# Kernel tuning notes

Hardware: AMD Instinct MI355X
Metric: run time of the kernel (lower is better)

Reference implementation:

```python
import jax, jax.numpy as jnp
from jax import lax
import numpy as np

ALPHA = 100.0  # NetVLAD beta

def _avg_pool2(x):
    # AvgPool2d(2, stride=2) on NCHW
    s = lax.reduce_window(x, 0.0, lax.add, (1, 1, 2, 2), (1, 1, 2, 2), 'VALID')
    return s * 0.25

def _conv3x3(x, w, b):
    y = lax.conv_general_dilated(x, w, (1, 1), 'SAME',
                                 dimension_numbers=('NCHW', 'OIHW', 'NCHW'))
    return y + b[None, :, None, None]

def _l2norm(v, axis):
    return v / jnp.maximum(jnp.linalg.norm(v, axis=axis, keepdims=True), 1e-12)


def setup_inputs() -> dict:
    key = jax.random.key(0)
    ks = jax.random.split(key, 10)
    N, H, W = 16, 512, 512
    K, D = 64, 16          # clusters, NetVLAD feature dim (conv2 out channels)
    T, E, Hd = 64, 300, 512  # caption len, emb dim (rnn_inp=rnn_out), rnn_hid
    img = jax.random.normal(ks[0], (N, 3, H, W), jnp.float32)
    cap = jax.random.normal(ks[1], (N, T, E), jnp.float32)
    conv1_w = jax.random.normal(ks[2], (4, 3, 3, 3), jnp.float32) * 0.1
    conv1_b = jnp.zeros((4,), jnp.float32)
    conv2_w = jax.random.normal(ks[3], (16, 4, 3, 3), jnp.float32) * 0.1
    conv2_b = jnp.zeros((16,), jnp.float32)
    centroids = jax.random.uniform(ks[4], (K, D), jnp.float32)  # torch.rand init
    nv_w = 2.0 * ALPHA * centroids                     # 1x1 conv weight, squeezed [K,D]
    nv_b = -ALPHA * jnp.linalg.norm(centroids, axis=1)  # [K]
    fc_w = jax.random.normal(ks[5], (Hd, K * D), jnp.float32) * 0.02
    fc_b = jnp.zeros((Hd,), jnp.float32)
    hid_w = jax.random.normal(ks[6], (Hd, E + Hd), jnp.float32) * 0.02
    hid_b = jnp.zeros((Hd,), jnp.float32)
    out_w = jax.random.normal(ks[7], (E, Hd), jnp.float32) * 0.02
    out_b = jnp.zeros((E,), jnp.float32)
    return dict(img=img, cap=cap, conv1_w=conv1_w, conv1_b=conv1_b,
                conv2_w=conv2_w, conv2_b=conv2_b, centroids=centroids,
                nv_w=nv_w, nv_b=nv_b, fc_w=fc_w, fc_b=fc_b,
                hid_w=hid_w, hid_b=hid_b, out_w=out_w, out_b=out_b)


def reference(img, cap, conv1_w, conv1_b, conv2_w, conv2_b, centroids,
              nv_w, nv_b, fc_w, fc_b, hid_w, hid_b, out_w, out_b):
    # CNN encoder
    x = jax.nn.relu(_conv3x3(img, conv1_w, conv1_b))
    x = _avg_pool2(x)
    x = jax.nn.relu(_conv3x3(x, conv2_w, conv2_b))
    x = _avg_pool2(x)                      # [N, 16, 128, 128]
    N, C = x.shape[0], x.shape[1]
    xf = x.reshape(N, C, -1)               # [N, C, HW]
    # NetVLAD: 1x1 conv -> softmax over clusters
    soft_assign = jnp.einsum('kc,nch->nkh', nv_w, xf) + nv_b[None, :, None]
    soft_assign = jax.nn.softmax(soft_assign, axis=1)  # [N, K, HW]
    # algebraic two-matmul form of sum_hw a[n,k,hw]*(x[n,c,hw]-centroids[k,c])
    a_sum = soft_assign.sum(axis=-1)                      # [N, K]
    vlad = jnp.einsum('nkh,nch->nkc', soft_assign, xf)    # [N, K, C]
    vlad = vlad - a_sum[:, :, None] * centroids[None]     # [N, K, C]
    vlad = _l2norm(vlad, axis=2)
    vlad = vlad.reshape(N, -1)
    vlad = _l2norm(vlad, axis=1)
    features = vlad @ fc_w.T + fc_b                        # [N, rnn_hid]
    # RNN decoder on sample 0
    feat0 = features[0]
    cap0 = cap[0]                                          # [T, E]

    def step(carry, x_t):
        h, x_in = carry
        comb = jnp.concatenate([x_in, h])
        h_new = jax.nn.sigmoid(hid_w @ comb + hid_b)
        y = jax.nn.sigmoid(out_w @ h_new + out_b)
        return (h_new, x_t), y

    (_, ys) = lax.scan(step, (feat0, cap0[0]), cap0[1:])
    output = jnp.concatenate([cap0[:1], ys], axis=0)       # [T, E]
    loss = jnp.mean((output - cap0) ** 2)
    return loss
```

## Files before the change

kernel.cpp:

```cpp
#include <hip/hip_runtime.h>
#include <math.h>


#define POISON 0xAAAAAAAAu
#define MAGIC  0x13579BDFu

__device__ __forceinline__ float sigmoidf_(float x) {
  return 1.0f / (1.0f + __expf(-x));
}
__device__ __forceinline__ unsigned uld(const unsigned* p) {
  return __hip_atomic_load(p, __ATOMIC_RELAXED, __HIP_MEMORY_SCOPE_AGENT);
}
__device__ __forceinline__ float fld(const float* p) {
  return __hip_atomic_load(p, __ATOMIC_RELAXED, __HIP_MEMORY_SCOPE_AGENT);
}
__device__ __forceinline__ void fst(float* p, float v) {
  __hip_atomic_store(p, v, __ATOMIC_RELAXED, __HIP_MEMORY_SCOPE_AGENT);
}
__device__ __forceinline__ void ust(unsigned* p, unsigned v) {
  __hip_atomic_store(p, v, __ATOMIC_RELAXED, __HIP_MEMORY_SCOPE_AGENT);
}

__global__ __launch_bounds__(256, 1)
void k_front(const float* __restrict__ img,  const float* __restrict__ cap,
             const float* __restrict__ c1w,  const float* __restrict__ c1b,
             const float* __restrict__ c2w,  const float* __restrict__ c2b,
             const float* __restrict__ cent, const float* __restrict__ nvw,
             const float* __restrict__ nvb,  const float* __restrict__ fcw,
             const float* __restrict__ fcb,  const float* __restrict__ hidw,
             const float* __restrict__ hidb,
             float* __restrict__ vacc, float* __restrict__ asum,
             float* __restrict__ feat, float* __restrict__ U,
             float* __restrict__ H,
             unsigned* __restrict__ flags, float* __restrict__ loss) {
  __shared__ __align__(16) float smem[19392];
  const int bx  = blockIdx.x;
  const int tid = threadIdx.x;
  unsigned* flag_magic = flags + 0;
  unsigned* vlad_done  = flags + 1;

  if (bx == 0) {
    for (int i = tid; i < 1024; i += 256) fst(vacc + i, 0.f);
    if (tid < 64) fst(asum + tid, 0.f);
    if (tid == 0) { fst(loss, 0.f); ust(vlad_done, 0u); }
    unsigned* Hu = (unsigned*)H;
    for (int i = tid; i < 63 * 512; i += 256) ust(Hu + i, POISON);
    __syncthreads();
    if (tid == 0) ust(flag_magic, MAGIC);
    return;
  }

  if (bx < 64) {
    const int t = bx - 1;
    float* csh = smem;
    if (tid < 256) csh[tid] = cap[t * 300 + tid];
    if (tid < 44) csh[256 + tid] = cap[t * 300 + 256 + tid];
    __syncthreads();
    #pragma unroll
    for (int rr = 0; rr < 2; ++rr) {
      int row = tid + rr * 256;
      float acc = hidb[row];
      const float4* w4 = (const float4*)(hidw + row * 812);
      const float4* c4 = (const float4*)csh;
      #pragma unroll 5
      for (int i = 0; i < 75; ++i) {
        float4 aa = w4[i]; float4 xx = c4[i];
        acc = fmaf(aa.x, xx.x, acc); acc = fmaf(aa.y, xx.y, acc);
        acc = fmaf(aa.z, xx.z, acc); acc = fmaf(aa.w, xx.w, acc);
      }
      U[t * 512 + row] = acc;
    }
    return;
  }

  if (bx < 72) {
    const int q = bx - 64;
    if (tid == 0) {
      while (uld(vlad_done) != 64u) __builtin_amdgcn_s_sleep(8);
    }
    __syncthreads();
    float* v  = smem;
    float* rn = smem + 1024;
    float* fr = smem + 1088;
    for (int i = tid; i < 1024; i += 256)
      v[i] = fld(vacc + i) - fld(asum + (i >> 4)) * cent[i];
    __syncthreads();
    if (tid < 64) {
      float ss = 0.f;
      #pragma unroll
      for (int c = 0; c < 16; ++c) { float xx = v[tid * 16 + c]; ss = fmaf(xx, xx, ss); }
      rn[tid] = fmaxf(sqrtf(ss), 1e-12f);
    }
    __syncthreads();
    float gs = 0.f;
    for (int i = tid; i < 1024; i += 256) {
      float nv = v[i] / rn[i >> 4];
      v[i] = nv;
      gs = fmaf(nv, nv, gs);
    }
    #pragma unroll
    for (int o = 32; o > 0; o >>= 1) gs += __shfl_down(gs, o);
    if ((tid & 63) == 0) fr[tid >> 6] = gs;
    __syncthreads();
    if (tid == 0) {
      float tot = fr[0] + fr[1] + fr[2] + fr[3];
      fr[8] = 1.0f / fmaxf(sqrtf(tot), 1e-12f);
    }
    __syncthreads();
    float invg = fr[8];
    int row = q * 64 + (tid >> 2);
    int cg = tid & 3;
    float acc = 0.f;
    const float4* fw4 = (const float4*)(fcw + row * 1024 + cg * 256);
    const float4* v4  = (const float4*)(v + cg * 256);
    #pragma unroll 4
    for (int i = 0; i < 64; ++i) {
      float4 aa = fw4[i]; float4 xx = v4[i];
      acc = fmaf(aa.x, xx.x, acc); acc = fmaf(aa.y, xx.y, acc);
      acc = fmaf(aa.z, xx.z, acc); acc = fmaf(aa.w, xx.w, acc);
    }
    acc += __shfl_xor(acc, 1);
    acc += __shfl_xor(acc, 2);
    if (cg == 0) feat[row] = fmaf(invg, acc, fcb[row]);
    return;
  }

  {
    const int vb = bx - 72;
    float* p1sh = smem;
    float* ps   = smem + 6336;
    float* xs   = smem + 14656;
    float* wsh  = smem + 17216;
    float* bsh  = smem + 18240;
    float* aS   = smem + 18304;
    float* cw2  = smem + 18560;
    float* cb2  = smem + 19136;
    float* cw1  = smem + 19152;
    float* cb1  = smem + 19260;
    for (int i = tid; i < 1024; i += 256) wsh[i] = nvw[i];
    if (tid < 64) bsh[tid] = nvb[tid];
    for (int i = tid; i < 576; i += 256) cw2[i] = c2w[i];
    if (tid < 16) cb2[tid] = c2b[tid];
    if (tid < 108) cw1[tid] = c1w[tid];
    if (tid >= 108 && tid < 112) cb1[tid - 108] = c1b[tid - 108];
    __syncthreads();

    for (int f = tid; f < 6192; f += 256) {
      int c  = f / 1548;
      int r0 = f - c * 1548;
      int j  = r0 / 258;
      int xx = r0 - j * 258;
      int gy = 4 * vb - 1 + j;
      int gx = xx - 1;
      float val = 0.f;
      if ((unsigned)gy < 256u && (unsigned)gx < 256u) {
        float bb = cb1[c];
        float a00 = bb, a01 = bb, a10 = bb, a11 = bb;
        int y0 = 2 * gy - 1, x0 = 2 * gx - 1;
        #pragma unroll
        for (int ci = 0; ci < 3; ++ci) {
          float P[4][4];
          #pragma unroll
          for (int jj = 0; jj < 4; ++jj) {
            int y = y0 + jj;
            #pragma unroll
            for (int ii = 0; ii < 4; ++ii) {
              int x = x0 + ii;
              bool ok = ((unsigned)y < 512u) && ((unsigned)x < 512u);
              P[jj][ii] = ok ? img[ci * 262144 + y * 512 + x] : 0.0f;
            }
          }
          #pragma unroll
          for (int ky = 0; ky < 3; ++ky) {
            #pragma unroll
            for (int kx = 0; kx < 3; ++kx) {
              float wv = cw1[c * 27 + ci * 9 + ky * 3 + kx];
              a00 = fmaf(wv, P[ky][kx],         a00);
              a01 = fmaf(wv, P[ky][kx + 1],     a01);
              a10 = fmaf(wv, P[ky + 1][kx],     a10);
              a11 = fmaf(wv, P[ky + 1][kx + 1], a11);
            }
          }
        }
        val = 0.25f * (fmaxf(a00, 0.f) + fmaxf(a01, 0.f) +
                       fmaxf(a10, 0.f) + fmaxf(a11, 0.f));
      }
      p1sh[c * 1584 + j * 264 + xx] = val;
    }
    __syncthreads();

    int ox = tid & 127;
    int oyl = tid >> 7;
    float a[16][4];
    #pragma unroll
    for (int oc = 0; oc < 16; ++oc) {
      float bb = cb2[oc];
      a[oc][0] = bb; a[oc][1] = bb; a[oc][2] = bb; a[oc][3] = bb;
    }
    #pragma unroll
    for (int ci = 0; ci < 4; ++ci) {
      float P[4][4];
      #pragma unroll
      for (int jj = 0; jj < 4; ++jj) {
        #pragma unroll
        for (int ii = 0; ii < 4; ++ii)
          P[jj][ii] = p1sh[ci * 1584 + (2 * oyl + jj) * 264 + 2 * ox + ii];
      }
      #pragma unroll
      for (int oc = 0; oc < 16; ++oc) {
        #pragma unroll
        for (int ky = 0; ky < 3; ++ky) {
          #pragma unroll
          for (int kx = 0; kx < 3; ++kx) {
            float wv = cw2[oc * 36 + ci * 9 + ky * 3 + kx];
            a[oc][0] = fmaf(wv, P[ky][kx],         a[oc][0]);
            a[oc][1] = fmaf(wv, P[ky][kx + 1],     a[oc][1]);
            a[oc][2] = fmaf(wv, P[ky + 1][kx],     a[oc][2]);
            a[oc][3] = fmaf(wv, P[ky + 1][kx + 1], a[oc][3]);
          }
        }
      }
    }
    float x[16];
    #pragma unroll
    for (int oc = 0; oc < 16; ++oc)
      x[oc] = 0.25f * (fmaxf(a[oc][0], 0.f) + fmaxf(a[oc][1], 0.f) +
                       fmaxf(a[oc][2], 0.f) + fmaxf(a[oc][3], 0.f));

    float p[64];
    float m = -1e30f;
    #pragma unroll
    for (int k = 0; k < 64; ++k) {
      float acc = bsh[k];
      #pragma unroll
      for (int c = 0; c < 16; ++c) acc = fmaf(wsh[k * 16 + c], x[c], acc);
      p[k] = acc;
      m = fmaxf(m, acc);
    }
    float s = 0.f;
    #pragma unroll
    for (int k = 0; k < 64; ++k) { p[k] = __expf(p[k] - m); s += p[k]; }
    float inv = 1.0f / s;
    #pragma unroll
    for (int k = 0; k < 64; ++k) p[k] *= inv;

    int q = tid >> 6, k = tid & 63;
    float acc[16];
    #pragma unroll
    for (int c = 0; c < 16; ++c) acc[c] = 0.f;
    float accA = 0.f;
    for (int pass = 0; pass < 2; ++pass) {
      __syncthreads();
      if ((tid >> 7) == pass) {
        int tt = tid & 127;
        #pragma unroll
        for (int kk = 0; kk < 64; ++kk) ps[tt * 65 + kk] = p[kk];
        #pragma unroll
        for (int c = 0; c < 16; ++c) xs[tt * 20 + c] = x[c];
      }
      __syncthreads();
      #pragma unroll
      for (int j = 0; j < 32; ++j) {
        int tt = q * 32 + j;
        float pv = ps[tt * 65 + k];
        accA += pv;
        const float4* xv = (const float4*)(xs + tt * 20);
        #pragma unroll
        for (int c4 = 0; c4 < 4; ++c4) {
          float4 xx = xv[c4];
          acc[c4 * 4 + 0] = fmaf(pv, xx.x, acc[c4 * 4 + 0]);
          acc[c4 * 4 + 1] = fmaf(pv, xx.y, acc[c4 * 4 + 1]);
          acc[c4 * 4 + 2] = fmaf(pv, xx.z, acc[c4 * 4 + 2]);
          acc[c4 * 4 + 3] = fmaf(pv, xx.w, acc[c4 * 4 + 3]);
        }
      }
    }
    __syncthreads();
    float* red = ps;
    #pragma unroll
    for (int c = 0; c < 16; ++c) red[tid * 16 + c] = acc[c];
    aS[tid] = accA;
    __syncthreads();
    if (tid == 0) {
      while (uld(flag_magic) != MAGIC) __builtin_amdgcn_s_sleep(2);
    }
    __syncthreads();
    if (q == 0) {
      float aa = aS[k] + aS[64 + k] + aS[128 + k] + aS[192 + k];
      atomicAdd(&asum[k], aa);
    }
    int k2 = tid >> 2;
    int cgc = (tid & 3) * 4;
    #pragma unroll
    for (int cc = 0; cc < 4; ++cc) {
      int c = cgc + cc;
      float vv = red[(0 * 64 + k2) * 16 + c] + red[(1 * 64 + k2) * 16 + c] +
                 red[(2 * 64 + k2) * 16 + c] + red[(3 * 64 + k2) * 16 + c];
      atomicAdd(&vacc[k2 * 16 + c], vv);
    }
    __syncthreads();
    if (tid == 0)
      __hip_atomic_fetch_add(vlad_done, 1u, __ATOMIC_RELAXED,
                             __HIP_MEMORY_SCOPE_AGENT);
  }
}

__global__ __launch_bounds__(512, 1)
void k_back(const float* __restrict__ hidw, const float* __restrict__ U,
            const float* __restrict__ feat, float* __restrict__ H,
            const float* __restrict__ outw, const float* __restrict__ outb,
            const float* __restrict__ cap,  float* __restrict__ loss) {
  __shared__ __align__(16) float smem[1100];
  const int bx  = blockIdx.x;
  const int tid = threadIdx.x;
  unsigned* Hu = (unsigned*)H;

  if (bx < 4) {
    const int r   = tid >> 2;
    const int cg  = tid & 3;
    const int row = bx * 128 + r;
    float wrf[128];
    {
      const float4* wp = (const float4*)(hidw + row * 812 + 300 + cg * 128);
      #pragma unroll
      for (int i = 0; i < 32; ++i) {
        float4 tm = wp[i];
        wrf[4 * i + 0] = tm.x; wrf[4 * i + 1] = tm.y;
        wrf[4 * i + 2] = tm.z; wrf[4 * i + 3] = tm.w;
      }
    }
    #pragma unroll
    for (int i = 0; i < 128; ++i) asm volatile("" : "+v"(wrf[i]));
    float* buf0 = smem;
    float* buf1 = smem + 544;
    const int wz = (tid >> 7) * 136 + (tid & 127);
    const int wown = ((row >> 7) * 136) + (row & 127);
    const bool own = ((tid >> 7) == bx);
    buf0[wz] = feat[tid];
    __syncthreads();
    for (int t = 0; t < 63; ++t) {
      const float* rb = ((t & 1) ? buf1 : buf0) + cg * 136;
      float uval = (cg == 0) ? U[t * 512 + row] : 0.f;
      float acc = 0.f;
      #pragma unroll
      for (int i = 0; i < 32; ++i) {
        float4 h4 = *(const float4*)(rb + i * 4);
        acc = fmaf(wrf[4 * i + 0], h4.x, acc);
        acc = fmaf(wrf[4 * i + 1], h4.y, acc);
        acc = fmaf(wrf[4 * i + 2], h4.z, acc);
        acc = fmaf(wrf[4 * i + 3], h4.w, acc);
      }
      acc += __shfl_xor(acc, 1);
      acc += __shfl_xor(acc, 2);
      float hn = 0.f;
      if (cg == 0) {
        hn = sigmoidf_(acc + uval);
        fst(H + t * 512 + row, hn);
      }
      if (t < 62) {
        float* bufn = (t & 1) ? buf0 : buf1;
        if (cg == 0) bufn[wown] = hn;
        if (!own) {
          const unsigned* src = Hu + t * 512 + tid;
          unsigned aa;
          do {
            aa = uld(src);
          } while (aa == POISON);
          bufn[wz] = __uint_as_float(aa);
        }
        __syncthreads();
      }
    }
    return;
  }

  const int t = bx - 4;
  float* hsh = smem;
  float* red = smem + 512;
  if (tid == 0) {
    while (uld(Hu + (size_t)t * 512) == POISON) __builtin_amdgcn_s_sleep(32);
  }
  __syncthreads();
  {
    const unsigned* src = Hu + (size_t)t * 512 + tid;
    unsigned aa;
    do {
      aa = uld(src);
    } while (aa == POISON);
    hsh[tid] = __uint_as_float(aa);
  }
  __syncthreads();
  float se = 0.f;
  if (tid < 300) {
    float acc = outb[tid];
    const float4* w4 = (const float4*)(outw + tid * 512);
    const float4* h4 = (const float4*)hsh;
    #pragma unroll 4
    for (int i = 0; i < 128; ++i) {
      float4 aa = w4[i]; float4 xx = h4[i];
      acc = fmaf(aa.x, xx.x, acc); acc = fmaf(aa.y, xx.y, acc);
      acc = fmaf(aa.z, xx.z, acc); acc = fmaf(aa.w, xx.w, acc);
    }
    float y = sigmoidf_(acc);
    float d = y - cap[(t + 1) * 300 + tid];
    se = fmaf(d, d, se);
  }
  #pragma unroll
  for (int o = 32; o > 0; o >>= 1) se += __shfl_down(se, o);
  if ((tid & 63) == 0) red[tid >> 6] = se;
  __syncthreads();
  if (tid == 0) {
    float tot = 0.f;
    #pragma unroll
    for (int qq = 0; qq < 8; ++qq) tot += red[qq];
    atomicAdd(loss, tot * (1.0f / 19200.0f));
  }
}

extern "C" void kernel_launch(void* const* d_in, const int* in_sizes, int n_in,
                              void* d_out, int out_size, void* d_ws, size_t ws_size,
                              hipStream_t stream) {
  (void)in_sizes; (void)n_in; (void)out_size; (void)ws_size;
  const float* img  = (const float*)d_in[0];
  const float* cap  = (const float*)d_in[1];
  const float* c1w  = (const float*)d_in[2];
  const float* c1b  = (const float*)d_in[3];
  const float* c2w  = (const float*)d_in[4];
  const float* c2b  = (const float*)d_in[5];
  const float* cent = (const float*)d_in[6];
  const float* nvw  = (const float*)d_in[7];
  const float* nvb  = (const float*)d_in[8];
  const float* fcw  = (const float*)d_in[9];
  const float* fcb  = (const float*)d_in[10];
  const float* hidw = (const float*)d_in[11];
  const float* hidb = (const float*)d_in[12];
  const float* outw = (const float*)d_in[13];
  const float* outb = (const float*)d_in[14];

  float* ws   = (float*)d_ws;
  float* vacc = ws;
  float* asum = ws + 1024;
  float* feat = ws + 1088;
  float* U    = ws + 1600;
  float* H    = ws + 33856;
  unsigned* flags = (unsigned*)(ws + 66112);

  k_front<<<136, 256, 0, stream>>>(img, cap, c1w, c1b, c2w, c2b, cent, nvw,
                                   nvb, fcw, fcb, hidw, hidb,
                                   vacc, asum, feat, U, H, flags,
                                   (float*)d_out);
  k_back<<<67, 512, 0, stream>>>(hidw, U, feat, H, outw, outb, cap,
                                 (float*)d_out);
}
```

Baseline: 287.8 us.

## Merge front and back kernels into one persistent kernel with flag-based handoff

Fuses the two launches into a single 108-block, 512-thread kernel. The image blocks now cover 8 rows each, so 32 VLAD blocks replace 64. The U-projection blocks also compute the output and loss, and the recurrence blocks spin on poisoned feat and U values instead of waiting for a kernel boundary. This removes one launch and the inter-kernel gap and lets the RNN recurrence start as soon as features are ready. It relies on all blocks being co-resident for the spin-waits, and halves the number of front-end blocks, which may lengthen the conv phase.

Measured after the change: 299.4 us. 4.0% more time.

```diff
diff --git a/kernel.cpp b/kernel.cpp
--- a/kernel.cpp
+++ b/kernel.cpp
@@ -21,136 +21,65 @@
   __hip_atomic_store(p, v, __ATOMIC_RELAXED, __HIP_MEMORY_SCOPE_AGENT);
 }
 
-__global__ __launch_bounds__(256, 1)
-void k_front(const float* __restrict__ img,  const float* __restrict__ cap,
-             const float* __restrict__ c1w,  const float* __restrict__ c1b,
-             const float* __restrict__ c2w,  const float* __restrict__ c2b,
-             const float* __restrict__ cent, const float* __restrict__ nvw,
-             const float* __restrict__ nvb,  const float* __restrict__ fcw,
-             const float* __restrict__ fcb,  const float* __restrict__ hidw,
-             const float* __restrict__ hidb,
-             float* __restrict__ vacc, float* __restrict__ asum,
-             float* __restrict__ feat, float* __restrict__ U,
-             float* __restrict__ H,
-             unsigned* __restrict__ flags, float* __restrict__ loss) {
-  __shared__ __align__(16) float smem[19392];
+__global__ __launch_bounds__(512, 1)
+void k_all(const float* __restrict__ img,  const float* __restrict__ cap,
+           const float* __restrict__ c1w,  const float* __restrict__ c1b,
+           const float* __restrict__ c2w,  const float* __restrict__ c2b,
+           const float* __restrict__ cent, const float* __restrict__ nvw,
+           const float* __restrict__ nvb,  const float* __restrict__ fcw,
+           const float* __restrict__ fcb,  const float* __restrict__ hidw,
+           const float* __restrict__ hidb, const float* __restrict__ outw,
+           const float* __restrict__ outb,
+           float* __restrict__ vacc, float* __restrict__ asum,
+           float* __restrict__ feat, float* __restrict__ U,
+           float* __restrict__ H,
+           unsigned* __restrict__ flags, float* __restrict__ loss) {
+  __shared__ __align__(16) float smem[23744];
   const int bx  = blockIdx.x;
   const int tid = threadIdx.x;
   unsigned* flag_magic = flags + 0;
   unsigned* vlad_done  = flags + 1;
 
   if (bx == 0) {
-    for (int i = tid; i < 1024; i += 256) fst(vacc + i, 0.f);
+    for (int i = tid; i < 1024; i += 512) fst(vacc + i, 0.f);
     if (tid < 64) fst(asum + tid, 0.f);
     if (tid == 0) { fst(loss, 0.f); ust(vlad_done, 0u); }
+    unsigned* Uu = (unsigned*)U;
     unsigned* Hu = (unsigned*)H;
-    for (int i = tid; i < 63 * 512; i += 256) ust(Hu + i, POISON);
+    unsigned* Fu = (unsigned*)feat;
+    for (int i = tid; i < 63 * 512; i += 512) { ust(Uu + i, POISON); ust(Hu + i, POISON); }
+    ust(Fu + tid, POISON);
     __syncthreads();
     if (tid == 0) ust(flag_magic, MAGIC);
     return;
   }
 
-  if (bx < 64) {
-    const int t = bx - 1;
-    float* csh = smem;
-    if (tid < 256) csh[tid] = cap[t * 300 + tid];
-    if (tid < 44) csh[256 + tid] = cap[t * 300 + 256 + tid];
-    __syncthreads();
-    #pragma unroll
-    for (int rr = 0; rr < 2; ++rr) {
-      int row = tid + rr * 256;
-      float acc = hidb[row];
-      const float4* w4 = (const float4*)(hidw + row * 812);
-      const float4* c4 = (const float4*)csh;
-      #pragma unroll 5
-      for (int i = 0; i < 75; ++i) {
-        float4 aa = w4[i]; float4 xx = c4[i];
-        acc = fmaf(aa.x, xx.x, acc); acc = fmaf(aa.y, xx.y, acc);
-        acc = fmaf(aa.z, xx.z, acc); acc = fmaf(aa.w, xx.w, acc);
-      }
-      U[t * 512 + row] = acc;
-    }
-    return;
-  }
-
-  if (bx < 72) {
-    const int q = bx - 64;
-    if (tid == 0) {
-      while (uld(vlad_done) != 64u) __builtin_amdgcn_s_sleep(8);
-    }
-    __syncthreads();
-    float* v  = smem;
-    float* rn = smem + 1024;
-    float* fr = smem + 1088;
-    for (int i = tid; i < 1024; i += 256)
-      v[i] = fld(vacc + i) - fld(asum + (i >> 4)) * cent[i];
-    __syncthreads();
-    if (tid < 64) {
-      float ss = 0.f;
-      #pragma unroll
-      for (int c = 0; c < 16; ++c) { float xx = v[tid * 16 + c]; ss = fmaf(xx, xx, ss); }
-      rn[tid] = fmaxf(sqrtf(ss), 1e-12f);
-    }
-    __syncthreads();
-    float gs = 0.f;
-    for (int i = tid; i < 1024; i += 256) {
-      float nv = v[i] / rn[i >> 4];
-      v[i] = nv;
-      gs = fmaf(nv, nv, gs);
-    }
-    #pragma unroll
-    for (int o = 32; o > 0; o >>= 1) gs += __shfl_down(gs, o);
-    if ((tid & 63) == 0) fr[tid >> 6] = gs;
-    __syncthreads();
-    if (tid == 0) {
-      float tot = fr[0] + fr[1] + fr[2] + fr[3];
-      fr[8] = 1.0f / fmaxf(sqrtf(tot), 1e-12f);
-    }
-    __syncthreads();
-    float invg = fr[8];
-    int row = q * 64 + (tid >> 2);
-    int cg = tid & 3;
-    float acc = 0.f;
-    const float4* fw4 = (const float4*)(fcw + row * 1024 + cg * 256);
-    const float4* v4  = (const float4*)(v + cg * 256);
-    #pragma unroll 4
-    for (int i = 0; i < 64; ++i) {
-      float4 aa = fw4[i]; float4 xx = v4[i];
-      acc = fmaf(aa.x, xx.x, acc); acc = fmaf(aa.y, xx.y, acc);
-      acc = fmaf(aa.z, xx.z, acc); acc = fmaf(aa.w, xx.w, acc);
-    }
-    acc += __shfl_xor(acc, 1);
-    acc += __shfl_xor(acc, 2);
-    if (cg == 0) feat[row] = fmaf(invg, acc, fcb[row]);
-    return;
-  }
-
-  {
-    const int vb = bx - 72;
+  if (bx < 33) {
+    const int vb = bx - 1;
     float* p1sh = smem;
-    float* ps   = smem + 6336;
-    float* xs   = smem + 14656;
-    float* wsh  = smem + 17216;
-    float* bsh  = smem + 18240;
-    float* aS   = smem + 18304;
-    float* cw2  = smem + 18560;
-    float* cb2  = smem + 19136;
-    float* cw1  = smem + 19152;
-    float* cb1  = smem + 19260;
-    for (int i = tid; i < 1024; i += 256) wsh[i] = nvw[i];
+    float* ps   = smem + 10560;
+    float* xs   = smem + 18880;
+    float* wsh  = smem + 21440;
+    float* bsh  = smem + 22464;
+    float* aS   = smem + 22528;
+    float* cw2  = smem + 23040;
+    float* cb2  = smem + 23616;
+    float* cw1  = smem + 23632;
+    float* cb1  = smem + 23740;
+    for (int i = tid; i < 1024; i += 512) wsh[i] = nvw[i];
     if (tid < 64) bsh[tid] = nvb[tid];
-    for (int i = tid; i < 576; i += 256) cw2[i] = c2w[i];
-    if (tid < 16) cb2[tid] = c2b[tid];
-    if (tid < 108) cw1[tid] = c1w[tid];
-    if (tid >= 108 && tid < 112) cb1[tid - 108] = c1b[tid - 108];
-    __syncthreads();
-
-    for (int f = tid; f < 6192; f += 256) {
-      int c  = f / 1548;
-      int r0 = f - c * 1548;
+    if (tid < 576) cw2[tid] = c2w[tid];
+    if (tid >= 576 && tid < 592) cb2[tid - 576] = c2b[tid - 576];
+    if (tid >= 592 && tid < 700) cw1[tid - 592] = c1w[tid - 592];
+    if (tid >= 700 && tid < 704) cb1[tid - 700] = c1b[tid - 700];
+    __syncthreads();
+
+    for (int f = tid; f < 10320; f += 512) {
+      int c  = f / 2580;
+      int r0 = f - c * 2580;
       int j  = r0 / 258;
       int xx = r0 - j * 258;
-      int gy = 4 * vb - 1 + j;
+      int gy = 8 * vb - 1 + j;
       int gx = xx - 1;
       float val = 0.f;
       if ((unsigned)gy < 256u && (unsigned)gx < 256u) {
@@ -185,7 +114,7 @@
         val = 0.25f * (fmaxf(a00, 0.f) + fmaxf(a01, 0.f) +
                        fmaxf(a10, 0.f) + fmaxf(a11, 0.f));
       }
-      p1sh[c * 1584 + j * 264 + xx] = val;
+      p1sh[c * 2640 + j * 264 + xx] = val;
     }
     __syncthreads();
 
@@ -204,7 +133,7 @@
       for (int jj = 0; jj < 4; ++jj) {
         #pragma unroll
         for (int ii = 0; ii < 4; ++ii)
-          P[jj][ii] = p1sh[ci * 1584 + (2 * oyl + jj) * 264 + 2 * ox + ii];
+          P[jj][ii] = p1sh[ci * 2640 + (2 * oyl + jj) * 264 + 2 * ox + ii];
       }
       #pragma unroll
       for (int oc = 0; oc < 16; ++oc) {
@@ -249,7 +178,7 @@
     #pragma unroll
     for (int c = 0; c < 16; ++c) acc[c] = 0.f;
     float accA = 0.f;
-    for (int pass = 0; pass < 2; ++pass) {
+    for (int pass = 0; pass < 4; ++pass) {
       __syncthreads();
       if ((tid >> 7) == pass) {
         int tt = tid & 127;
@@ -260,8 +189,8 @@
       }
       __syncthreads();
       #pragma unroll
-      for (int j = 0; j < 32; ++j) {
-        int tt = q * 32 + j;
+      for (int j = 0; j < 16; ++j) {
+        int tt = q * 16 + j;
         float pv = ps[tt * 65 + k];
         accA += pv;
         const float4* xv = (const float4*)(xs + tt * 20);
@@ -286,39 +215,88 @@
     }
     __syncthreads();
     if (q == 0) {
-      float aa = aS[k] + aS[64 + k] + aS[128 + k] + aS[192 + k];
+      float aa = 0.f;
+      #pragma unroll
+      for (int qq = 0; qq < 8; ++qq) aa += aS[qq * 64 + k];
       atomicAdd(&asum[k], aa);
     }
-    int k2 = tid >> 2;
-    int cgc = (tid & 3) * 4;
-    #pragma unroll
-    for (int cc = 0; cc < 4; ++cc) {
-      int c = cgc + cc;
-      float vv = red[(0 * 64 + k2) * 16 + c] + red[(1 * 64 + k2) * 16 + c] +
-                 red[(2 * 64 + k2) * 16 + c] + red[(3 * 64 + k2) * 16 + c];
+    int k2 = tid >> 3;
+    int c0 = (tid & 7) * 2;
+    #pragma unroll
+    for (int cc = 0; cc < 2; ++cc) {
+      int c = c0 + cc;
+      float vv = 0.f;
+      #pragma unroll
+      for (int qq = 0; qq < 8; ++qq) vv += red[(qq * 64 + k2) * 16 + c];
       atomicAdd(&vacc[k2 * 16 + c], vv);
     }
     __syncthreads();
     if (tid == 0)
       __hip_atomic_fetch_add(vlad_done, 1u, __ATOMIC_RELAXED,
                              __HIP_MEMORY_SCOPE_AGENT);
+    return;
   }
-}
-
-__global__ __launch_bounds__(512, 1)
-void k_back(const float* __restrict__ hidw, const float* __restrict__ U,
-            const float* __restrict__ feat, float* __restrict__ H,
-            const float* __restrict__ outw, const float* __restrict__ outb,
-            const float* __restrict__ cap,  float* __restrict__ loss) {
-  __shared__ __align__(16) float smem[1100];
-  const int bx  = blockIdx.x;
-  const int tid = threadIdx.x;
-  unsigned* Hu = (unsigned*)H;
-
-  if (bx < 4) {
+
+  if (bx < 41) {
+    const int q = bx - 33;
+    if (tid == 0) {
+      while (uld(vlad_done) != 32u) __builtin_amdgcn_s_sleep(8);
+    }
+    __syncthreads();
+    float* v  = smem;
+    float* rn = smem + 1024;
+    float* fr = smem + 1088;
+    for (int i = tid; i < 1024; i += 512)
+      v[i] = fld(vacc + i) - fld(asum + (i >> 4)) * cent[i];
+    __syncthreads();
+    if (tid < 64) {
+      float ss = 0.f;
+      #pragma unroll
+      for (int c = 0; c < 16; ++c) { float xx = v[tid * 16 + c]; ss = fmaf(xx, xx, ss); }
+      rn[tid] = fmaxf(sqrtf(ss), 1e-12f);
+    }
+    __syncthreads();
+    float gs = 0.f;
+    for (int i = tid; i < 1024; i += 512) {
+      float nv = v[i] / rn[i >> 4];
+      v[i] = nv;
+      gs = fmaf(nv, nv, gs);
+    }
+    #pragma unroll
+    for (int o = 32; o > 0; o >>= 1) gs += __shfl_down(gs, o);
+    if ((tid & 63) == 0) fr[tid >> 6] = gs;
+    __syncthreads();
+    if (tid == 0) {
+      float tot = 0.f;
+      #pragma unroll
+      for (int qq = 0; qq < 8; ++qq) tot += fr[qq];
+      fr[8] = 1.0f / fmaxf(sqrtf(tot), 1e-12f);
+    }
+    __syncthreads();
+    float invg = fr[8];
+    int row = q * 64 + (tid >> 3);
+    int cch = tid & 7;
+    float acc = 0.f;
+    const float4* fw4 = (const float4*)(fcw + row * 1024 + cch * 128);
+    const float4* v4  = (const float4*)(v + cch * 128);
+    #pragma unroll 4
+    for (int i = 0; i < 32; ++i) {
+      float4 aa = fw4[i]; float4 xx = v4[i];
+      acc = fmaf(aa.x, xx.x, acc); acc = fmaf(aa.y, xx.y, acc);
+      acc = fmaf(aa.z, xx.z, acc); acc = fmaf(aa.w, xx.w, acc);
+    }
+    acc += __shfl_down(acc, 4, 8);
+    acc += __shfl_down(acc, 2, 8);
+    acc += __shfl_down(acc, 1, 8);
+    if (cch == 0) fst(feat + row, fmaf(invg, acc, fcb[row]));
+    return;
+  }
+
+  if (bx < 45) {
+    const int rb_ = bx - 41;
     const int r   = tid >> 2;
     const int cg  = tid & 3;
-    const int row = bx * 128 + r;
+    const int row = rb_ * 128 + r;
     float wrf[128];
     {
       const float4* wp = (const float4*)(hidw + row * 812 + 300 + cg * 128);
@@ -329,22 +307,26 @@
         wrf[4 * i + 2] = tm.z; wrf[4 * i + 3] = tm.w;
       }
     }
-    #pragma unroll
-    for (int i = 0; i < 128; ++i) asm volatile("" : "+v"(wrf[i]));
     float* buf0 = smem;
     float* buf1 = smem + 544;
     const int wz = (tid >> 7) * 136 + (tid & 127);
     const int wown = ((row >> 7) * 136) + (row & 127);
-    const bool own = ((tid >> 7) == bx);
-    buf0[wz] = feat[tid];
+    const bool own = ((tid >> 7) == rb_);
+    unsigned* Hu = (unsigned*)H;
+    {
+      const unsigned* fu = (const unsigned*)feat + tid;
+      unsigned aa;
+      do { aa = uld(fu); } while (aa == POISON);
+      buf0[wz] = __uint_as_float(aa);
+    }
+    unsigned upat = (cg == 0) ? uld((const unsigned*)(U + row)) : 0u;
     __syncthreads();
     for (int t = 0; t < 63; ++t) {
-      const float* rb = ((t & 1) ? buf1 : buf0) + cg * 136;
-      float uval = (cg == 0) ? U[t * 512 + row] : 0.f;
+      const float* rbp = ((t & 1) ? buf1 : buf0) + cg * 136;
       float acc = 0.f;
       #pragma unroll
       for (int i = 0; i < 32; ++i) {
-        float4 h4 = *(const float4*)(rb + i * 4);
+        float4 h4 = *(const float4*)(rbp + i * 4);
         acc = fmaf(wrf[4 * i + 0], h4.x, acc);
         acc = fmaf(wrf[4 * i + 1], h4.y, acc);
         acc = fmaf(wrf[4 * i + 2], h4.z, acc);
@@ -354,18 +336,20 @@
       acc += __shfl_xor(acc, 2);
       float hn = 0.f;
       if (cg == 0) {
-        hn = sigmoidf_(acc + uval);
+        while (upat == POISON) upat = uld((const unsigned*)(U + t * 512 + row));
+        hn = sigmoidf_(acc + __uint_as_float(upat));
         fst(H + t * 512 + row, hn);
       }
       if (t < 62) {
         float* bufn = (t & 1) ? buf0 : buf1;
-        if (cg == 0) bufn[wown] = hn;
+        if (cg == 0) {
+          bufn[wown] = hn;
+          upat = uld((const unsigned*)(U + (t + 1) * 512 + row));
+        }
         if (!own) {
           const unsigned* src = Hu + t * 512 + tid;
           unsigned aa;
-          do {
-            aa = uld(src);
-          } while (aa == POISON);
+          do { aa = uld(src); } while (aa == POISON);
           bufn[wz] = __uint_as_float(aa);
         }
         __syncthreads();
@@ -374,46 +358,67 @@
     return;
   }
 
-  const int t = bx - 4;
-  float* hsh = smem;
-  float* red = smem + 512;
-  if (tid == 0) {
-    while (uld(Hu + (size_t)t * 512) == POISON) __builtin_amdgcn_s_sleep(32);
-  }
-  __syncthreads();
   {
-    const unsigned* src = Hu + (size_t)t * 512 + tid;
-    unsigned aa;
-    do {
-      aa = uld(src);
-    } while (aa == POISON);
-    hsh[tid] = __uint_as_float(aa);
-  }
-  __syncthreads();
-  float se = 0.f;
-  if (tid < 300) {
-    float acc = outb[tid];
-    const float4* w4 = (const float4*)(outw + tid * 512);
-    const float4* h4 = (const float4*)hsh;
-    #pragma unroll 4
-    for (int i = 0; i < 128; ++i) {
-      float4 aa = w4[i]; float4 xx = h4[i];
-      acc = fmaf(aa.x, xx.x, acc); acc = fmaf(aa.y, xx.y, acc);
-      acc = fmaf(aa.z, xx.z, acc); acc = fmaf(aa.w, xx.w, acc);
-    }
-    float y = sigmoidf_(acc);
-    float d = y - cap[(t + 1) * 300 + tid];
-    se = fmaf(d, d, se);
-  }
-  #pragma unroll
-  for (int o = 32; o > 0; o >>= 1) se += __shfl_down(se, o);
-  if ((tid & 63) == 0) red[tid >> 6] = se;
-  __syncthreads();
-  if (tid == 0) {
-    float tot = 0.f;
-    #pragma unroll
-    for (int qq = 0; qq < 8; ++qq) tot += red[qq];
-    atomicAdd(loss, tot * (1.0f / 19200.0f));
+    const int t = bx - 45;
+    unsigned* Hu = (unsigned*)H;
+    if (tid == 0) {
+      while (uld(flag_magic) != MAGIC) __builtin_amdgcn_s_sleep(8);
+    }
+    __syncthreads();
+    float* csh = smem;
+    if (tid < 300) csh[tid] = cap[t * 300 + tid];
+    __syncthreads();
+    {
+      float acc = hidb[tid];
+      const float4* w4 = (const float4*)(hidw + tid * 812);
+      const float4* c4 = (const float4*)csh;
+      #pragma unroll 5
+      for (int i = 0; i < 75; ++i) {
+        float4 aa = w4[i]; float4 xx = c4[i];
+        acc = fmaf(aa.x, xx.x, acc); acc = fmaf(aa.y, xx.y, acc);
+        acc = fmaf(aa.z, xx.z, acc); acc = fmaf(aa.w, xx.w, acc);
+      }
+      fst(U + t * 512 + tid, acc);
+    }
+    __syncthreads();
+    if (tid == 0) {
+      while (uld(Hu + (size_t)t * 512) == POISON) __builtin_amdgcn_s_sleep(64);
+    }
+    __syncthreads();
+    float* hsh = smem;
+    float* red = smem + 512;
+    {
+      const unsigned* src = Hu + (size_t)t * 512 + tid;
+      unsigned aa;
+      do { aa = uld(src); } while (aa == POISON);
+      hsh[tid] = __uint_as_float(aa);
+    }
+    __syncthreads();
+    float se = 0.f;
+    if (tid < 300) {
+      float acc = outb[tid];
+      const float4* w4 = (const float4*)(outw + tid * 512);
+      const float4* h4 = (const float4*)hsh;
+      #pragma unroll 4
+      for (int i = 0; i < 128; ++i) {
+        float4 aa = w4[i]; float4 xx = h4[i];
+        acc = fmaf(aa.x, xx.x, acc); acc = fmaf(aa.y, xx.y, acc);
+        acc = fmaf(aa.z, xx.z, acc); acc = fmaf(aa.w, xx.w, acc);
+      }
+      float y = sigmoidf_(acc);
+      float d = y - cap[(t + 1) * 300 + tid];
+      se = fmaf(d, d, se);
+    }
+    #pragma unroll
+    for (int o = 32; o > 0; o >>= 1) se += __shfl_down(se, o);
+    if ((tid & 63) == 0) red[tid >> 6] = se;
+    __syncthreads();
+    if (tid == 0) {
+      float tot = 0.f;
+      #pragma unroll
+      for (int qq = 0; qq < 8; ++qq) tot += red[qq];
+      atomicAdd(loss, tot * (1.0f / 19200.0f));
+    }
   }
 }
 
@@ -445,10 +450,8 @@
   float* H    = ws + 33856;
   unsigned* flags = (unsigned*)(ws + 66112);
 
-  k_front<<<136, 256, 0, stream>>>(img, cap, c1w, c1b, c2w, c2b, cent, nvw,
-                                   nvb, fcw, fcb, hidw, hidb,
-                                   vacc, asum, feat, U, H, flags,
-                                   (float*)d_out);
-  k_back<<<67, 512, 0, stream>>>(hidw, U, feat, H, outw, outb, cap,
+  k_all<<<108, 512, 0, stream>>>(img, cap, c1w, c1b, c2w, c2b, cent, nvw,
+                                 nvb, fcw, fcb, hidw, hidb, outw, outb,
+                                 vacc, asum, feat, U, H, flags,
                                  (float*)d_out);
 }
```
